# Kernel optimization log

Measured on AMD Instinct MI355X. Metric: run time of the kernel, lower is better.

The kernel has to match this reference:

```python
import jax, jax.numpy as jnp
import numpy as np

NMS_THRESHOLD = 0.7
PROPOSAL_COUNT = 1000   # post-NMS ROIs
PRE_NMS_LIMIT = 6000    # top-k anchors kept before NMS
BBOX_STD_DEV = np.array([0.1, 0.1, 0.2, 0.2], dtype=np.float32)
NEG = -1e9              # suppressed-score sentinel


def setup_inputs() -> dict:
    key = jax.random.key(0)
    k1, k2, k3, k4 = jax.random.split(key, 4)
    B, N = 8, 261888
    # [B, N, 2] background/foreground probabilities
    rpn_probs = jax.nn.softmax(jax.random.normal(k1, (B, N, 2), dtype=jnp.float32), axis=-1)
    # [B, N, 4] box refinement deltas (dy, dx, log(dh), log(dw)), pre-std-dev scaling
    rpn_bbox = jax.random.normal(k2, (B, N, 4), dtype=jnp.float32)
    # [B, N, 4] valid normalized anchors (y1, x1, y2, x2)
    ctr = jax.random.uniform(k3, (B, N, 2), minval=0.05, maxval=0.95)
    size = jax.random.uniform(k4, (B, N, 2), minval=0.02, maxval=0.3)
    anchors = jnp.clip(jnp.concatenate([ctr - 0.5 * size, ctr + 0.5 * size], axis=-1), 0.0, 1.0)
    return {"rpn_probs": rpn_probs, "rpn_bbox": rpn_bbox, "anchors": anchors}


def apply_box_deltas(boxes, deltas):
    # boxes: [..., 4] (y1,x1,y2,x2); deltas: [..., 4] (dy,dx,dlogh,dlogw)
    h = boxes[..., 2] - boxes[..., 0]
    w = boxes[..., 3] - boxes[..., 1]
    cy = boxes[..., 0] + 0.5 * h + deltas[..., 0] * h
    cx = boxes[..., 1] + 0.5 * w + deltas[..., 1] * w
    h = h * jnp.exp(deltas[..., 2])
    w = w * jnp.exp(deltas[..., 3])
    y1 = cy - 0.5 * h
    x1 = cx - 0.5 * w
    return jnp.stack([y1, x1, y1 + h, x1 + w], axis=-1)


def nms_pad(boxes, scores):
    # Greedy NMS for one image. boxes: [K,4], scores: [K].
    # Returns [PROPOSAL_COUNT, 4], zero-padded (matches tf.image.non_max_suppression + pad).
    area = (boxes[:, 2] - boxes[:, 0]) * (boxes[:, 3] - boxes[:, 1])

    def step(sc, _):
        i = jnp.argmax(sc)
        valid = sc[i] > NEG * 0.5
        b = boxes[i]
        iy1 = jnp.maximum(b[0], boxes[:, 0])
        ix1 = jnp.maximum(b[1], boxes[:, 1])
        iy2 = jnp.minimum(b[2], boxes[:, 2])
        ix2 = jnp.minimum(b[3], boxes[:, 3])
        inter = jnp.maximum(iy2 - iy1, 0.0) * jnp.maximum(ix2 - ix1, 0.0)
        iou = inter / (area[i] + area - inter + 1e-12)
        sc = jnp.where(iou > NMS_THRESHOLD, NEG, sc)
        sc = sc.at[i].set(NEG)  # always remove the selected box
        return sc, (i, valid)

    _, (idx, valid) = jax.lax.scan(step, scores, None, length=PROPOSAL_COUNT)
    return boxes[idx] * valid.astype(boxes.dtype)[:, None]


def reference(rpn_probs, rpn_bbox, anchors):
    # Foreground scores
    scores = rpn_probs[..., 1]                                   # [B, N]
    deltas = rpn_bbox * jnp.asarray(BBOX_STD_DEV)                # [B, N, 4]
    N = scores.shape[1]
    k = min(PRE_NMS_LIMIT, N)
    top_scores, ix = jax.lax.top_k(scores, k)                    # [B, k]
    deltas_k = jnp.take_along_axis(deltas, ix[..., None], axis=1)   # [B, k, 4]
    anchors_k = jnp.take_along_axis(anchors, ix[..., None], axis=1) # [B, k, 4]
    # Decode and clip to the [0,1] normalized window
    boxes = jnp.clip(apply_box_deltas(anchors_k, deltas_k), 0.0, 1.0)
    # Per-image NMS, padded to PROPOSAL_COUNT
    proposals = jax.vmap(nms_pad)(boxes, top_scores)             # [B, PROPOSAL_COUNT, 4]
    return proposals
```

## Files before the change

kernel.cpp:

```cpp
#include <hip/hip_runtime.h>

#pragma clang fp contract(off)

#define NB 8
#define KSEL 6000
#define KPAD 6016
#define PROP 1000
#define NTILE 94
#define RMAX 2048
#define RTILES 32
#define SWORDS 32
#define EQ2CAP 262144

#define OFF_HIST1 0u
#define OFF_CTRL  131072u
#define OFF_SEL   131584u
#define OFF_EQ2   516608u
#define OFF_BOX   17293824u
#define OFF_MAT   18063872u
#define MAT_BYTES 4194304ull

struct Ctrl {
  unsigned t1, rem1, selCount, eqCount, total;
  unsigned pad[11];
};

__global__ __launch_bounds__(256) void zero_kernel(unsigned* p, int n) {
  int i = blockIdx.x * 256 + threadIdx.x;
  if (i < n) p[i] = 0u;
}

__global__ __launch_bounds__(256) void hist12_kernel(const float* __restrict__ probs,
                                                     unsigned* __restrict__ hist, int N) {
  __shared__ unsigned lh[4096];
  const int b = blockIdx.y;
  for (int k = threadIdx.x; k < 4096; k += 256) lh[k] = 0u;
  __syncthreads();
  const int start = blockIdx.x * 2048;
  const int end = min(start + 2048, N);
#pragma unroll
  for (int j = 0; j < 4; ++j) {
    const int i = start + j * 512 + (int)threadIdx.x * 2;
    if (i < end) {
      const float4 p2 = *(const float4*)(probs + ((size_t)b * N + i) * 2);
      atomicAdd(&lh[__float_as_uint(p2.y) >> 20], 1u);
      if (i + 1 < end) atomicAdd(&lh[__float_as_uint(p2.w) >> 20], 1u);
    }
  }
  __syncthreads();
  for (int k = threadIdx.x; k < 4096; k += 256) {
    const unsigned v = lh[k];
    if (v) atomicAdd(&hist[b * 4096 + k], v);
  }
}

__global__ __launch_bounds__(64) void scan12_kernel(const unsigned* __restrict__ hist,
                                                    Ctrl* __restrict__ ctrl) {
  const int b = blockIdx.x;
  const int lane = threadIdx.x;
  const unsigned target = (unsigned)KSEL;
  const unsigned* h = hist + b * 4096;
  const int topbin = 4095 - lane * 64;
  unsigned mysum = 0;
  for (int c = 0; c < 64; c++) mysum += h[topbin - c];
  unsigned cum = mysum;
  for (int off = 1; off < 64; off <<= 1) {
    const unsigned v = __shfl_up(cum, off, 64);
    if (lane >= off) cum += v;
  }
  const unsigned prev = cum - mysum;
  if (prev < target && cum >= target) {
    unsigned c2 = prev;
    for (int c = 0; c < 64; c++) {
      const int bin = topbin - c;
      const unsigned hv = h[bin];
      if (c2 + hv >= target) { ctrl[b].t1 = (unsigned)bin; ctrl[b].rem1 = target - c2; break; }
      c2 += hv;
    }
  }
}

__global__ __launch_bounds__(256) void compact2_kernel(const float* __restrict__ probs,
                                                       Ctrl* __restrict__ ctrl,
                                                       unsigned long long* __restrict__ sel,
                                                       unsigned long long* __restrict__ eq2, int N) {
  __shared__ unsigned long long buf[2048];
  __shared__ unsigned s_ngt, s_neq, s_gbase, s_ebase;
  const int b = blockIdx.y;
  const int tid = threadIdx.x;
  const unsigned t1 = ctrl[b].t1;
  const int start = blockIdx.x * 2048;
  const int end = min(start + 2048, N);
  if (tid == 0) { s_ngt = 0u; s_neq = 0u; }
  __syncthreads();
  unsigned bits[8];
  int idxs[8];
#pragma unroll
  for (int j = 0; j < 4; ++j) {
    const int i = start + j * 512 + tid * 2;
    float4 p2 = make_float4(0.f, 0.f, 0.f, 0.f);
    if (i < end) p2 = *(const float4*)(probs + ((size_t)b * N + i) * 2);
    bits[j * 2]     = (i < end) ? __float_as_uint(p2.y) : 0u;
    idxs[j * 2]     = (i < end) ? i : -1;
    bits[j * 2 + 1] = (i + 1 < end) ? __float_as_uint(p2.w) : 0u;
    idxs[j * 2 + 1] = (i + 1 < end) ? (i + 1) : -1;
  }
#pragma unroll
  for (int e = 0; e < 8; ++e) {
    if (idxs[e] >= 0) {
      const unsigned top = bits[e] >> 20;
      if (top > t1) {
        const unsigned p = atomicAdd(&s_ngt, 1u);
        buf[p] = ((unsigned long long)bits[e] << 32) | (unsigned)idxs[e];
      } else if (top == t1) {
        const unsigned p = atomicAdd(&s_neq, 1u);
        buf[2047 - p] = ((unsigned long long)bits[e] << 32) | (unsigned)idxs[e];
      }
    }
  }
  __syncthreads();
  const unsigned ngt = s_ngt, neq = s_neq;
  if (tid == 0 && ngt) s_gbase = atomicAdd(&ctrl[b].selCount, ngt);
  if (tid == 1 && neq) s_ebase = atomicAdd(&ctrl[b].eqCount, neq);
  __syncthreads();
  for (unsigned k = tid; k < ngt; k += 256) {
    const unsigned p = s_gbase + k;
    if (p < (unsigned)KPAD) sel[b * KPAD + p] = buf[k];
  }
  for (unsigned k = tid; k < neq; k += 256) {
    const unsigned p = s_ebase + k;
    if (p < (unsigned)EQ2CAP) eq2[(size_t)b * EQ2CAP + p] = buf[2047 - k];
  }
}

__device__ inline void scan1024_desc(const unsigned* h, unsigned target, int lane,
                                     unsigned* outBin, unsigned* outRem) {
  const int topbin = 1023 - lane * 16;
  unsigned mysum = 0;
  for (int c = 0; c < 16; ++c) mysum += h[topbin - c];
  unsigned cum = mysum;
  for (int off = 1; off < 64; off <<= 1) {
    const unsigned v = __shfl_up(cum, off, 64);
    if (lane >= off) cum += v;
  }
  const unsigned prev = cum - mysum;
  if (prev < target && cum >= target) {
    unsigned c2 = prev;
    for (int c = 0; c < 16; ++c) {
      const int bin = topbin - c;
      const unsigned hv = h[bin];
      if (c2 + hv >= target) { *outBin = (unsigned)bin; *outRem = target - c2; break; }
      c2 += hv;
    }
  }
}
__device__ inline void scan1024_asc(const unsigned* h, unsigned target, int lane,
                                    unsigned* outBin, unsigned* outRem) {
  const int botbin = lane * 16;
  unsigned mysum = 0;
  for (int c = 0; c < 16; ++c) mysum += h[botbin + c];
  unsigned cum = mysum;
  for (int off = 1; off < 64; off <<= 1) {
    const unsigned v = __shfl_up(cum, off, 64);
    if (lane >= off) cum += v;
  }
  const unsigned prev = cum - mysum;
  if (prev < target && cum >= target) {
    unsigned c2 = prev;
    for (int c = 0; c < 16; ++c) {
      const int bin = botbin + c;
      const unsigned hv = h[bin];
      if (c2 + hv >= target) { *outBin = (unsigned)bin; *outRem = target - c2; break; }
      c2 += hv;
    }
  }
}

__global__ __launch_bounds__(256) void eqres2_kernel(Ctrl* __restrict__ ctrl,
                                                     const unsigned long long* __restrict__ eq2,
                                                     unsigned long long* __restrict__ sel) {
  __shared__ unsigned h1[1024];
  __shared__ unsigned s_binA, s_remA, s_binB, s_remB, s_binC, s_remC;
  __shared__ unsigned s_pos, s_lcnt;
  __shared__ unsigned s_lidx[256];
  const int b = blockIdx.x;
  const int tid = threadIdx.x, lane = tid & 63, wv = tid >> 6;
  unsigned cnt = ctrl[b].eqCount; if (cnt > (unsigned)EQ2CAP) cnt = EQ2CAP;
  const unsigned rem1 = ctrl[b].rem1;
  const unsigned long long* E = eq2 + (size_t)b * EQ2CAP;

  for (int k = tid; k < 1024; k += 256) h1[k] = 0u;
  __syncthreads();
  for (unsigned k = tid; k < cnt; k += 256)
    atomicAdd(&h1[((unsigned)(E[k] >> 32) >> 10) & 1023u], 1u);
  __syncthreads();
  if (wv == 0) scan1024_desc(h1, rem1, lane, &s_binA, &s_remA);
  __syncthreads();
  const unsigned binA = s_binA, remA = s_remA;
  __syncthreads();
  for (int k = tid; k < 1024; k += 256) h1[k] = 0u;
  __syncthreads();
  for (unsigned k = tid; k < cnt; k += 256) {
    const unsigned bits = (unsigned)(E[k] >> 32);
    if (((bits >> 10) & 1023u) == binA) atomicAdd(&h1[bits & 1023u], 1u);
  }
  __syncthreads();
  if (wv == 0) scan1024_desc(h1, remA, lane, &s_binB, &s_remB);
  __syncthreads();
  const unsigned binB = s_binB, remB = s_remB;
  const unsigned key20 = (binA << 10) | binB;
  __syncthreads();
  for (int k = tid; k < 1024; k += 256) h1[k] = 0u;
  __syncthreads();
  for (unsigned k = tid; k < cnt; k += 256) {
    const unsigned long long r = E[k];
    if (((unsigned)(r >> 32) & 0xFFFFFu) == key20) atomicAdd(&h1[((unsigned)r) >> 8], 1u);
  }
  __syncthreads();
  if (wv == 0) scan1024_asc(h1, remB, lane, &s_binC, &s_remC);
  if (tid == 0) { s_pos = ctrl[b].selCount; s_lcnt = 0u; }
  __syncthreads();
  const unsigned binC = s_binC, remC = s_remC;
  for (unsigned k0 = 0; k0 < cnt; k0 += 256) {
    const unsigned k = k0 + tid;
    bool take = false, lst = false;
    unsigned long long rec = 0ull;
    if (k < cnt) {
      rec = E[k];
      const unsigned bits = (unsigned)(rec >> 32);
      const unsigned k20 = bits & 0xFFFFFu;
      const unsigned idx = (unsigned)rec;
      if ((k20 >> 10) > binA) take = true;
      else if ((k20 >> 10) == binA && (k20 & 1023u) > binB) take = true;
      else if (k20 == key20) {
        if ((idx >> 8) < binC) take = true;
        else if ((idx >> 8) == binC) lst = true;
      }
    }
    const unsigned long long mt = __ballot(take);
    if (mt) {
      const int leader = __builtin_ctzll(mt);
      unsigned base = 0;
      if (lane == leader) base = atomicAdd(&s_pos, (unsigned)__builtin_popcountll(mt));
      base = (unsigned)__shfl((int)base, leader, 64);
      if (take) {
        const int rk = __builtin_popcountll(mt & ((1ull << lane) - 1ull));
        const unsigned p = base + (unsigned)rk;
        if (p < (unsigned)KPAD) sel[b * KPAD + p] = rec;
      }
    }
    if (lst) {
      const unsigned p = atomicAdd(&s_lcnt, 1u);
      if (p < 256u) s_lidx[p] = (unsigned)rec;
    }
  }
  __syncthreads();
  const unsigned lcnt = (s_lcnt < 256u) ? s_lcnt : 256u;
  const unsigned long long thrHi = ((unsigned long long)((ctrl[b].t1 << 20) | key20)) << 32;
  if (tid < (int)lcnt) {
    const unsigned my = s_lidx[tid];
    unsigned rk = 0;
    for (unsigned f = 0; f < lcnt; ++f) rk += (s_lidx[f] < my) ? 1u : 0u;
    if (rk < remC) {
      const unsigned p = atomicAdd(&s_pos, 1u);
      if (p < (unsigned)KPAD) sel[b * KPAD + p] = thrHi | (unsigned long long)my;
    }
  }
  __syncthreads();
  if (tid == 0) ctrl[b].total = s_pos;
}

__global__ __launch_bounds__(256) void rank_kernel(const Ctrl* __restrict__ ctrl,
                                                   const unsigned long long* __restrict__ sel,
                                                   const float* __restrict__ anchors,
                                                   const float* __restrict__ bbox,
                                                   float4* __restrict__ boxes, int N) {
  const int b = blockIdx.x & 7;
  const int it = blockIdx.x >> 3;
  const int tid = threadIdx.x;
  const int wv = tid >> 6, lane = tid & 63;
  __shared__ unsigned long long skey[KPAD];
  __shared__ unsigned scnt[4][64];
  int total = (int)ctrl[b].total; if (total > KSEL) total = KSEL;
  for (int i = tid; i < KPAD; i += 256) {
    unsigned long long kp = 0ull;
    if (i < total) {
      const unsigned long long e = sel[b * KPAD + i];
      kp = (e & 0xFFFFFFFF00000000ull) | (unsigned long long)(0xFFFFFFFFu - (unsigned)e);
    }
    skey[i] = kp;
  }
  __syncthreads();
  const int me = it * 64 + lane;
  const unsigned long long myk = skey[me];
  const int chunk = KPAD / 4;
  const int lo = wv * chunk;
  unsigned cnt = 0;
#pragma unroll 8
  for (int c = 0; c < chunk; ++c) cnt += (skey[lo + c] > myk) ? 1u : 0u;
  scnt[wv][lane] = cnt;
  __syncthreads();
  if (wv == 0 && me < total) {
    const unsigned rank = scnt[0][lane] + scnt[1][lane] + scnt[2][lane] + scnt[3][lane];
    unsigned idx = 0xFFFFFFFFu - (unsigned)myk;
    if (idx >= (unsigned)N) idx = 0;
    const float4 A = ((const float4*)anchors)[(size_t)b * N + idx];
    const float4 R = ((const float4*)bbox)[(size_t)b * N + idx];
    const float d0 = R.x * 0.1f, d1 = R.y * 0.1f, d2 = R.z * 0.2f, d3 = R.w * 0.2f;
    const float h = A.z - A.x;
    const float w = A.w - A.y;
    const float cy = A.x + 0.5f * h + d0 * h;
    const float cx = A.y + 0.5f * w + d1 * w;
    const float e2 = (float)exp((double)d2);
    const float e3 = (float)exp((double)d3);
    const float h2 = h * e2;
    const float w2 = w * e3;
    float y1 = cy - 0.5f * h2;
    float x1 = cx - 0.5f * w2;
    float y2 = y1 + h2;
    float x2 = x1 + w2;
    y1 = fminf(fmaxf(y1, 0.0f), 1.0f);
    x1 = fminf(fmaxf(x1, 0.0f), 1.0f);
    y2 = fminf(fmaxf(y2, 0.0f), 1.0f);
    x2 = fminf(fmaxf(x2, 0.0f), 1.0f);
    boxes[b * KPAD + rank] = make_float4(y1, x1, y2, x2);
  }
}

__global__ __launch_bounds__(256) void suppmat_kernel(const float4* __restrict__ boxes,
                                                      unsigned long long* __restrict__ mat) {
  const int b = blockIdx.x & 7;
  int t = blockIdx.x >> 3;
  int it = 0, rem = SWORDS;
  while (t >= rem) { t -= rem; ++it; rem = SWORDS - it; }
  const int jt = it + t;
  const int wv = threadIdx.x >> 6;
  const int lane = threadIdx.x & 63;
  const float4* gbox = boxes + b * KPAD;
  __shared__ float4 srow[64];
  __shared__ float sarea[64];
  if (threadIdx.x < 64) {
    const float4 v = gbox[it * 64 + threadIdx.x];
    srow[threadIdx.x] = v;
    sarea[threadIdx.x] = (v.z - v.x) * (v.w - v.y);
  }
  const int c = jt * 64 + lane;
  const float4 cv = gbox[c];
  const float ca = (cv.z - cv.x) * (cv.w - cv.y);
  __syncthreads();
  const double M = 0.7000000178813934326171875;
  unsigned long long* obase = mat + ((size_t)b * RMAX + (size_t)it * 64) * SWORDS + jt;
#pragma unroll
  for (int k = 0; k < 16; ++k) {
    const int r = wv * 16 + k;
    const int i = it * 64 + r;
    const float4 hb = srow[r];
    const float ha = sarea[r];
    const float iy1 = fmaxf(hb.x, cv.x);
    const float ix1 = fmaxf(hb.y, cv.y);
    const float iy2 = fminf(hb.z, cv.z);
    const float ix2 = fminf(hb.w, cv.w);
    const float dy = fmaxf(iy2 - iy1, 0.0f);
    const float dx = fmaxf(ix2 - ix1, 0.0f);
    const float inter = dy * dx;
    const float denom = ha + ca - inter + 1e-12f;
    const bool s = (c > i) && ((double)inter >= M * (double)denom);
    const unsigned long long w = __ballot(s);
    if (lane == 0) obase[(size_t)r * SWORDS] = w;
  }
}

__global__ __launch_bounds__(64) void nmsscan_kernel(const Ctrl* __restrict__ ctrl,
                                                     const float4* __restrict__ boxes,
                                                     const unsigned long long* __restrict__ mat,
                                                     float* __restrict__ out) {
  const int b = blockIdx.x;
  const int lane = threadIdx.x;
  int total = (int)ctrl[b].total; if (total > KSEL) total = KSEL;
  const unsigned long long* rmat = mat + (size_t)b * RMAX * SWORDS;
  const float4* gbox = boxes + b * KPAD;
  float4* outv = (float4*)(out + (size_t)b * PROP * 4);
  __shared__ int s_sel[PROP];
  __shared__ float4 s_hbox[PROP];
  const int lim = (total < RMAX) ? total : RMAX;
  const int nchunks = (lim + 63) >> 6;
  const bool wlane = lane < SWORDS;
  unsigned long long r0 = 0ull;
  int nsel = 0;

  unsigned long long diagN = (lane < lim) ? rmat[(size_t)lane * SWORDS] : 0ull;
  for (int c = 0; c < nchunks && nsel < PROP; ++c) {
    const int base = c << 6;
    const int n = ((lim - base) < 64) ? (lim - base) : 64;
    const unsigned long long diag = diagN;
    const int nb2 = base + 64;
    diagN = ((c + 1) < nchunks && (nb2 + lane) < lim)
              ? rmat[(size_t)(nb2 + lane) * SWORDS + (c + 1)] : 0ull;
    unsigned long long aw = ~__shfl(r0, c, 64);
    if (n < 64) aw &= ((1ull << n) - 1ull);
    unsigned long long S = __ballot(diag != 0ull);
    while (S) {
      const int s = __builtin_ctzll(S);
      S &= S - 1ull;
      const unsigned long long cm = __shfl(diag, s, 64);
      if ((aw >> s) & 1ull) aw &= ~cm;
    }
    unsigned long long acc = aw;
    const int need = PROP - nsel;
    int na = __popcll(acc);
    if (na > need) {
      unsigned long long t2 = acc, a2 = 0ull;
      for (int c2 = 0; c2 < need; ++c2) { a2 |= t2 & (0ull - t2); t2 &= t2 - 1ull; }
      acc = a2; na = need;
    }
    if ((acc >> lane) & 1ull) {
      const int r = __popcll(acc & ((1ull << lane) - 1ull));
      s_sel[nsel + r] = base + lane;
    }
    nsel += na;
    if (nsel >= PROP || c + 1 >= nchunks) continue;
    if (wlane) {
      const unsigned long long* rowbase = rmat + (size_t)base * SWORDS + lane;
      unsigned long long o = 0ull;
#pragma unroll
      for (int r = 0; r < 64; ++r) {
        const unsigned long long v = rowbase[(size_t)r * SWORDS];
        o |= (((acc >> r) & 1ull) ? v : 0ull);
      }
      r0 |= o;
    }
  }
  if (nsel < PROP && total > lim) {
    for (int k = lane; k < nsel; k += 64) s_hbox[k] = gbox[s_sel[k]];
    __syncthreads();
    const double M = 0.7000000178813934326171875;
    for (int i2 = lim; i2 < total && nsel < PROP; ++i2) {
      const float4 v = gbox[i2];
      const float a = (v.z - v.x) * (v.w - v.y);
      bool supp = false;
      for (int h = lane; h < nsel; h += 64) {
        const float4 hb = s_hbox[h];
        const float ha = (hb.z - hb.x) * (hb.w - hb.y);
        const float iy1 = fmaxf(hb.x, v.x);
        const float ix1 = fmaxf(hb.y, v.y);
        const float iy2 = fminf(hb.z, v.z);
        const float ix2 = fminf(hb.w, v.w);
        const float dy = fmaxf(iy2 - iy1, 0.0f);
        const float dx = fmaxf(ix2 - ix1, 0.0f);
        const float inter = dy * dx;
        const float denom = ha + a - inter + 1e-12f;
        if ((double)inter >= M * (double)denom) { supp = true; break; }
      }
      if (!__any(supp)) {
        if (lane == 0) { s_sel[nsel] = i2; s_hbox[nsel] = v; }
        ++nsel;
      }
    }
  }
  __syncthreads();
  for (int k = lane; k < PROP; k += 64)
    outv[k] = (k < nsel) ? gbox[s_sel[k]] : make_float4(0.f, 0.f, 0.f, 0.f);
}

__global__ __launch_bounds__(1024) void nms_kernel(const float4* __restrict__ boxes, float* __restrict__ out) {
  const int b = blockIdx.x;
  const int tid = threadIdx.x;
  const int lane = tid & 63;
  const float4* gbox = boxes + b * KPAD;
  float* outB = out + b * (PROP * 4);
  __shared__ unsigned long long smask[94];
  __shared__ int s_widx[64];
  __shared__ float4 s_wbox[64];
  __shared__ float s_wha[64];
  __shared__ int s_cnt, s_nAcc, s_total, s_cursor;
  for (int k = tid; k < 94; k += 1024)
    smask[k] = (k == 93) ? ((1ull << 48) - 1ull) : ~0ull;
  if (tid == 0) { s_cursor = 0; s_total = 0; }
  __syncthreads();
  const double M = 0.7000000178813934326171875;
  for (int round = 0; round < PROP; ++round) {
    if (tid == 0) {
      int cnt = 0;
      const int cur = s_cursor;
      int w = cur >> 6;
      unsigned long long word = (w < 94) ? (smask[w] & (~0ull << (cur & 63))) : 0ull;
      while (cnt < 64) {
        while (word == 0ull && ++w < 94) word = smask[w];
        if (w >= 94) break;
        const int bit = __builtin_ctzll(word);
        word &= word - 1ull;
        s_widx[cnt++] = (w << 6) | bit;
      }
      s_cnt = cnt;
      s_cursor = cnt ? (s_widx[cnt - 1] + 1) : KSEL;
    }
    __syncthreads();
    const int cnt = s_cnt;
    const int tailStart = s_cursor;
    if (cnt == 0) break;
    if (tid < 64) {
      const int j = (lane < cnt) ? s_widx[lane] : -1;
      float4 v = make_float4(0.f, 0.f, 0.f, 0.f);
      if (j >= 0) v = gbox[j];
      const float a = (v.z - v.x) * (v.w - v.y);
      const int totalOld = s_total;
      unsigned long long aliveW = __ballot(j >= 0);
      unsigned long long acc = 0ull;
      for (int i = 0; i < 64; ++i) {
        const float hx = __shfl(v.x, i), hy = __shfl(v.y, i);
        const float hz = __shfl(v.z, i), hw = __shfl(v.w, i);
        const float ha = __shfl(a, i);
        bool s = false;
        if (j >= 0 && lane > i) {
          const float iy1 = fmaxf(hx, v.x);
          const float ix1 = fmaxf(hy, v.y);
          const float iy2 = fminf(hz, v.z);
          const float ix2 = fminf(hw, v.w);
          const float dy = fmaxf(iy2 - iy1, 0.0f);
          const float dx = fmaxf(ix2 - ix1, 0.0f);
          const float inter = dy * dx;
          const float denom = ha + a - inter + 1e-12f;
          s = ((double)inter >= M * (double)denom);
        }
        const unsigned long long m = __ballot(s);
        if (aliveW & (1ull << i)) { acc |= 1ull << i; aliveW &= ~m; }
      }
      const int need = PROP - totalOld;
      int na = __popcll(acc);
      if (na > need) {
        unsigned long long t = acc, a2 = 0ull;
        for (int c2 = 0; c2 < need; ++c2) { a2 |= t & (0ull - t); t &= t - 1ull; }
        acc = a2; na = need;
      }
      if ((acc >> lane) & 1ull) {
        const int r = __popcll(acc & ((1ull << lane) - 1ull));
        float* o = outB + (size_t)(totalOld + r) * 4;
        o[0] = v.x; o[1] = v.y; o[2] = v.z; o[3] = v.w;
        s_wbox[r] = v; s_wha[r] = a;
      }
      if (lane == 0) { s_nAcc = na; s_total = totalOld + na; }
      if (j >= 0) atomicAnd(&smask[j >> 6], ~(1ull << (j & 63)));
    }
    __syncthreads();
    const int total = s_total;
    const int nAcc = s_nAcc;
    if (total >= PROP) break;
    for (int j = tailStart + tid; j < KSEL; j += 1024) {
      if (!((smask[j >> 6] >> (j & 63)) & 1ull)) continue;
      const float4 v = gbox[j];
      const float a = (v.z - v.x) * (v.w - v.y);
      bool supp = false;
      for (int r = 0; r < nAcc; ++r) {
        const float4 hb = s_wbox[r];
        const float ha = s_wha[r];
        const float iy1 = fmaxf(hb.x, v.x);
        const float ix1 = fmaxf(hb.y, v.y);
        const float iy2 = fminf(hb.z, v.z);
        const float ix2 = fminf(hb.w, v.w);
        const float dy = fmaxf(iy2 - iy1, 0.0f);
        const float dx = fmaxf(ix2 - ix1, 0.0f);
        const float inter = dy * dx;
        const float denom = ha + a - inter + 1e-12f;
        if ((double)inter >= M * (double)denom) { supp = true; break; }
      }
      if (supp) atomicAnd(&smask[j >> 6], ~(1ull << (j & 63)));
    }
    __syncthreads();
  }
  const int written = s_total;
  for (int u = written * 4 + tid; u < PROP * 4; u += 1024) outB[u] = 0.0f;
}

extern "C" void kernel_launch(void* const* d_in, const int* in_sizes, int n_in,
                              void* d_out, int out_size, void* d_ws, size_t ws_size,
                              hipStream_t stream) {
  (void)n_in; (void)out_size;
  const float* probs = (const float*)d_in[0];
  const float* bbox = (const float*)d_in[1];
  const float* anchors = (const float*)d_in[2];
  float* out = (float*)d_out;
  char* ws = (char*)d_ws;
  const int N = in_sizes[0] / (NB * 2);

  unsigned* hist1 = (unsigned*)(ws + OFF_HIST1);
  Ctrl* ctrl = (Ctrl*)(ws + OFF_CTRL);
  unsigned long long* sel = (unsigned long long*)(ws + OFF_SEL);
  unsigned long long* eq2 = (unsigned long long*)(ws + OFF_EQ2);
  float4* boxes = (float4*)(ws + OFF_BOX);
  unsigned long long* mat = (unsigned long long*)(ws + OFF_MAT);

  const int zeroN = (int)((OFF_SEL - OFF_HIST1) / 4);
  zero_kernel<<<dim3((zeroN + 255) / 256), dim3(256), 0, stream>>>((unsigned*)ws, zeroN);

  const int gx = (N + 2047) / 2048;
  hist12_kernel<<<dim3(gx, NB), dim3(256), 0, stream>>>(probs, hist1, N);
  scan12_kernel<<<dim3(NB), dim3(64), 0, stream>>>(hist1, ctrl);
  compact2_kernel<<<dim3(gx, NB), dim3(256), 0, stream>>>(probs, ctrl, sel, eq2, N);
  eqres2_kernel<<<dim3(NB), dim3(256), 0, stream>>>(ctrl, eq2, sel);
  rank_kernel<<<dim3(NTILE * NB), dim3(256), 0, stream>>>(ctrl, sel, anchors, bbox, boxes, N);

  if (ws_size >= (size_t)OFF_MAT + MAT_BYTES) {
    suppmat_kernel<<<dim3((SWORDS * (SWORDS + 1) / 2) * NB), dim3(256), 0, stream>>>(boxes, mat);
    nmsscan_kernel<<<dim3(NB), dim3(64), 0, stream>>>(ctrl, boxes, mat, out);
  } else {
    nms_kernel<<<dim3(NB), dim3(1024), 0, stream>>>(boxes, out);
  }
}
```

Measured before the change: 138.6 us.

## Add shared-memory rank fast path for top-k ties and transpose suppression matrix

```diff
diff --git a/kernel.cpp b/kernel.cpp
--- a/kernel.cpp
+++ b/kernel.cpp
@@ -6,11 +6,11 @@
 #define KSEL 6000
 #define KPAD 6016
 #define PROP 1000
+#define RMAX 2048
+#define SWORDS 32
 #define NTILE 94
-#define RMAX 2048
-#define RTILES 32
-#define SWORDS 32
 #define EQ2CAP 262144
+#define SUBCAP 1536
 
 #define OFF_HIST1 0u
 #define OFF_CTRL  131072u
@@ -180,8 +180,9 @@
                                                      const unsigned long long* __restrict__ eq2,
                                                      unsigned long long* __restrict__ sel) {
   __shared__ unsigned h1[1024];
+  __shared__ unsigned long long s_sub[SUBCAP];
   __shared__ unsigned s_binA, s_remA, s_binB, s_remB, s_binC, s_remC;
-  __shared__ unsigned s_pos, s_lcnt;
+  __shared__ unsigned s_pos, s_subcnt, s_lcnt;
   __shared__ unsigned s_lidx[256];
   const int b = blockIdx.x;
   const int tid = threadIdx.x, lane = tid & 63, wv = tid >> 6;
@@ -195,9 +196,57 @@
     atomicAdd(&h1[((unsigned)(E[k] >> 32) >> 10) & 1023u], 1u);
   __syncthreads();
   if (wv == 0) scan1024_desc(h1, rem1, lane, &s_binA, &s_remA);
+  if (tid == 0) { s_pos = ctrl[b].selCount; s_subcnt = 0u; }
   __syncthreads();
   const unsigned binA = s_binA, remA = s_remA;
-  __syncthreads();
+  for (unsigned k0 = 0; k0 < cnt; k0 += 256) {
+    const unsigned k = k0 + tid;
+    bool take = false, sub = false;
+    unsigned long long rec = 0ull;
+    if (k < cnt) {
+      rec = E[k];
+      const unsigned bk = ((unsigned)(rec >> 32) >> 10) & 1023u;
+      take = bk > binA;
+      sub = bk == binA;
+    }
+    const unsigned long long mt = __ballot(take);
+    if (mt) {
+      const int leader = __builtin_ctzll(mt);
+      unsigned base = 0;
+      if (lane == leader) base = atomicAdd(&s_pos, (unsigned)__builtin_popcountll(mt));
+      base = (unsigned)__shfl((int)base, leader, 64);
+      if (take) {
+        const int rk = __builtin_popcountll(mt & ((1ull << lane) - 1ull));
+        const unsigned p = base + (unsigned)rk;
+        if (p < (unsigned)KPAD) sel[b * KPAD + p] = rec;
+      }
+    }
+    if (sub) {
+      const unsigned p = atomicAdd(&s_subcnt, 1u);
+      if (p < (unsigned)SUBCAP) s_sub[p] = rec;
+    }
+  }
+  __syncthreads();
+  const unsigned subcnt = s_subcnt;
+  const unsigned base = s_pos;
+  if (subcnt <= (unsigned)SUBCAP) {
+    for (unsigned e = tid; e < subcnt; e += 256) {
+      const unsigned long long re = s_sub[e];
+      const unsigned long long ke = (re & 0xFFFFFFFF00000000ull) |
+                                    (unsigned long long)(0xFFFFFFFFu - (unsigned)re);
+      unsigned rk = 0;
+      for (unsigned f = 0; f < subcnt; ++f) {
+        const unsigned long long rf = s_sub[f];
+        const unsigned long long kf = (rf & 0xFFFFFFFF00000000ull) |
+                                      (unsigned long long)(0xFFFFFFFFu - (unsigned)rf);
+        rk += (kf > ke) ? 1u : 0u;
+      }
+      if (rk < remA) sel[b * KPAD + base + rk] = re;
+    }
+    __syncthreads();
+    if (tid == 0) ctrl[b].total = base + remA;
+    return;
+  }
   for (int k = tid; k < 1024; k += 256) h1[k] = 0u;
   __syncthreads();
   for (unsigned k = tid; k < cnt; k += 256) {
@@ -218,7 +267,7 @@
   }
   __syncthreads();
   if (wv == 0) scan1024_asc(h1, remB, lane, &s_binC, &s_remC);
-  if (tid == 0) { s_pos = ctrl[b].selCount; s_lcnt = 0u; }
+  if (tid == 0) s_lcnt = 0u;
   __syncthreads();
   const unsigned binC = s_binC, remC = s_remC;
   for (unsigned k0 = 0; k0 < cnt; k0 += 256) {
@@ -230,22 +279,23 @@
       const unsigned bits = (unsigned)(rec >> 32);
       const unsigned k20 = bits & 0xFFFFFu;
       const unsigned idx = (unsigned)rec;
-      if ((k20 >> 10) > binA) take = true;
-      else if ((k20 >> 10) == binA && (k20 & 1023u) > binB) take = true;
-      else if (k20 == key20) {
-        if ((idx >> 8) < binC) take = true;
-        else if ((idx >> 8) == binC) lst = true;
+      if ((k20 >> 10) == binA) {
+        if ((k20 & 1023u) > binB) take = true;
+        else if (k20 == key20) {
+          if ((idx >> 8) < binC) take = true;
+          else if ((idx >> 8) == binC) lst = true;
+        }
       }
     }
     const unsigned long long mt = __ballot(take);
     if (mt) {
       const int leader = __builtin_ctzll(mt);
-      unsigned base = 0;
-      if (lane == leader) base = atomicAdd(&s_pos, (unsigned)__builtin_popcountll(mt));
-      base = (unsigned)__shfl((int)base, leader, 64);
+      unsigned bs = 0;
+      if (lane == leader) bs = atomicAdd(&s_pos, (unsigned)__builtin_popcountll(mt));
+      bs = (unsigned)__shfl((int)bs, leader, 64);
       if (take) {
         const int rk = __builtin_popcountll(mt & ((1ull << lane) - 1ull));
-        const unsigned p = base + (unsigned)rk;
+        const unsigned p = bs + (unsigned)rk;
         if (p < (unsigned)KPAD) sel[b * KPAD + p] = rec;
       }
     }
@@ -339,6 +389,7 @@
   const float4* gbox = boxes + b * KPAD;
   __shared__ float4 srow[64];
   __shared__ float sarea[64];
+  __shared__ unsigned long long wrow[64];
   if (threadIdx.x < 64) {
     const float4 v = gbox[it * 64 + threadIdx.x];
     srow[threadIdx.x] = v;
@@ -349,7 +400,6 @@
   const float ca = (cv.z - cv.x) * (cv.w - cv.y);
   __syncthreads();
   const double M = 0.7000000178813934326171875;
-  unsigned long long* obase = mat + ((size_t)b * RMAX + (size_t)it * 64) * SWORDS + jt;
 #pragma unroll
   for (int k = 0; k < 16; ++k) {
     const int r = wv * 16 + k;
@@ -366,8 +416,11 @@
     const float denom = ha + ca - inter + 1e-12f;
     const bool s = (c > i) && ((double)inter >= M * (double)denom);
     const unsigned long long w = __ballot(s);
-    if (lane == 0) obase[(size_t)r * SWORDS] = w;
-  }
+    if (lane == 0) wrow[r] = w;
+  }
+  __syncthreads();
+  if (threadIdx.x < 64)
+    mat[((size_t)(b * SWORDS) + jt) * RMAX + (size_t)it * 64 + threadIdx.x] = wrow[threadIdx.x];
 }
 
 __global__ __launch_bounds__(64) void nmsscan_kernel(const Ctrl* __restrict__ ctrl,
@@ -377,7 +430,7 @@
   const int b = blockIdx.x;
   const int lane = threadIdx.x;
   int total = (int)ctrl[b].total; if (total > KSEL) total = KSEL;
-  const unsigned long long* rmat = mat + (size_t)b * RMAX * SWORDS;
+  const unsigned long long* cmat = mat + (size_t)(b * SWORDS) * RMAX;
   const float4* gbox = boxes + b * KPAD;
   float4* outv = (float4*)(out + (size_t)b * PROP * 4);
   __shared__ int s_sel[PROP];
@@ -388,14 +441,14 @@
   unsigned long long r0 = 0ull;
   int nsel = 0;
 
-  unsigned long long diagN = (lane < lim) ? rmat[(size_t)lane * SWORDS] : 0ull;
+  unsigned long long diagN = (lane < lim) ? cmat[lane] : 0ull;
   for (int c = 0; c < nchunks && nsel < PROP; ++c) {
     const int base = c << 6;
     const int n = ((lim - base) < 64) ? (lim - base) : 64;
     const unsigned long long diag = diagN;
     const int nb2 = base + 64;
     diagN = ((c + 1) < nchunks && (nb2 + lane) < lim)
-              ? rmat[(size_t)(nb2 + lane) * SWORDS + (c + 1)] : 0ull;
+              ? cmat[(size_t)(c + 1) * RMAX + nb2 + lane] : 0ull;
     unsigned long long aw = ~__shfl(r0, c, 64);
     if (n < 64) aw &= ((1ull << n) - 1ull);
     unsigned long long S = __ballot(diag != 0ull);
@@ -420,12 +473,13 @@
     nsel += na;
     if (nsel >= PROP || c + 1 >= nchunks) continue;
     if (wlane) {
-      const unsigned long long* rowbase = rmat + (size_t)base * SWORDS + lane;
+      const ulonglong2* ub = (const ulonglong2*)(cmat + (size_t)lane * RMAX + base);
       unsigned long long o = 0ull;
 #pragma unroll
-      for (int r = 0; r < 64; ++r) {
-        const unsigned long long v = rowbase[(size_t)r * SWORDS];
-        o |= (((acc >> r) & 1ull) ? v : 0ull);
+      for (int g = 0; g < 32; ++g) {
+        const ulonglong2 v = ub[g];
+        o |= (((acc >> (2 * g)) & 1ull) ? v.x : 0ull);
+        o |= (((acc >> (2 * g + 1)) & 1ull) ? v.y : 0ull);
       }
       r0 |= o;
     }
```

Result: faster. 122.5 us (-11.6%).
